# Kernel optimization log

Hardware: AMD Instinct MI355X
Metric: run time of the kernel (lower is better)

The kernel has to match this reference:

```python
import jax, jax.numpy as jnp
import numpy as np

B, L, G, D = 4096, 64, 8, 128
N_ITEMS, N_USERS, N_RATINGS = 100000, 50000, 5


def setup_inputs() -> dict:
    key = jax.random.key(0)
    ks = jax.random.split(key, 16)
    s = jnp.float32(0.02)
    return dict(
        nodes=jax.random.randint(ks[0], (B, G), 0, N_USERS),
        history_u=jax.random.randint(ks[1], (B, L), 0, N_ITEMS),
        history_r=jax.random.randint(ks[2], (B, L), 0, N_RATINGS),
        hist_len=jax.random.randint(ks[3], (B,), 0, L),
        v2e_weight=jax.random.normal(ks[4], (N_ITEMS, D), dtype=jnp.float32) * s,
        u2e_weight=jax.random.normal(ks[5], (N_USERS, D), dtype=jnp.float32) * s,
        r2e_weight=jax.random.normal(ks[6], (N_RATINGS, D), dtype=jnp.float32) * s,
        W1=jax.random.normal(ks[7], (2 * D, D), dtype=jnp.float32) * s,
        b1=jnp.zeros((D,), jnp.float32),
        W2=jax.random.normal(ks[8], (D, D), dtype=jnp.float32) * s,
        b2=jnp.zeros((D,), jnp.float32),
        att1_W=jax.random.normal(ks[9], (2 * D, D), dtype=jnp.float32) * s,
        att1_b=jnp.zeros((D,), jnp.float32),
        att2_W=jax.random.normal(ks[10], (D, D), dtype=jnp.float32) * s,
        att2_b=jnp.zeros((D,), jnp.float32),
        att3_W=jax.random.normal(ks[11], (D, 1), dtype=jnp.float32) * s,
        att3_b=jnp.zeros((1,), jnp.float32),
        ge_W=jax.random.normal(ks[12], (D, D), dtype=jnp.float32) * s,
        ge_b=jnp.zeros((D,), jnp.float32),
    )


def reference(nodes, history_u, history_r, hist_len,
              v2e_weight, u2e_weight, r2e_weight,
              W1, b1, W2, b2,
              att1_W, att1_b, att2_W, att2_b, att3_W, att3_b,
              ge_W, ge_b):
    lengths = hist_len + 1                      # ensure >=1 valid history entry per group
    e_uv = v2e_weight[history_u]                # [B, L, D] item-history gather
    e_r = r2e_weight[history_r]                 # [B, L, D] rating gather
    members = u2e_weight[nodes]                 # [B, G, D] member gather
    # Group_Embedding: pool members to one rep per group
    g = jax.nn.relu(members.mean(axis=1) @ ge_W + ge_b)            # [B, D]
    # per-history 2-layer MLP (w_r1, w_r2)
    x = jax.nn.relu(jnp.concatenate([e_uv, e_r], axis=-1) @ W1 + b1)
    o = jax.nn.relu(x @ W2 + b2)                # [B, L, D] o_history
    # Attention: cat(o_history, group_rep) -> relu -> relu -> scalar, softmax over L
    g_rep = jnp.broadcast_to(g[:, None, :], o.shape)               # [B, L, D]
    a = jax.nn.relu(jnp.concatenate([o, g_rep], axis=-1) @ att1_W + att1_b)
    a = jax.nn.relu(a @ att2_W + att2_b)
    logits = (a @ att3_W + att3_b)[..., 0]      # [B, L]
    mask = jnp.arange(L)[None, :] < lengths[:, None]
    logits = jnp.where(mask, logits, jnp.float32(-1e9))
    att = jax.nn.softmax(logits, axis=-1) * mask                   # ragged masked softmax
    # torch.mm(o_history.t(), att_w).t() == attention-weighted reduce over L
    return jnp.einsum('bl,bld->bd', att, o)     # [B, D]
```

## Files before the change

kernel.cpp:

```cpp
#include <hip/hip_runtime.h>
#include <hip/hip_bf16.h>

#define DD 128
#define TILE_BYTES 32768
#define WS_R_OFF   196608
#define WS_GB_OFF  199168

typedef __attribute__((ext_vector_type(8))) short bf16x8;
typedef __attribute__((ext_vector_type(4))) float f32x4;

__device__ inline unsigned short f2bf(float f) {
  unsigned u = __float_as_uint(f);
  return (unsigned short)((u + 0x7fffu + ((u >> 16) & 1u)) >> 16);
}
__device__ inline float bf2f(unsigned short h) {
  return __uint_as_float(((unsigned)h) << 16);
}

__device__ inline void async16(void* ldsp, const void* gp) {
  __builtin_amdgcn_global_load_lds(
      (const __attribute__((address_space(1))) void*)gp,
      (__attribute__((address_space(3))) void*)ldsp, 16, 0, 0);
}

__device__ inline void fill_w(char* slot, const char* src, int tid) {
  int w = tid >> 6, lane = tid & 63;
  #pragma unroll
  for (int i = 0; i < 8; ++i) {
    int ofs = ((i << 2) + w) << 10;
    async16(slot + ofs, src + ofs + lane * 16);
  }
}

__device__ inline bf16x8 ldfrag(const char* buf, int rowbase, int kk, int lane) {
  int row = rowbase + (lane & 15);
  int off = (row << 8) + (kk << 6) + (lane & 48);
  off ^= (row & 7) << 4;
  return *(const bf16x8*)(buf + off);
}

__device__ inline bf16x8 ldAg(const float* rp, int kk, int lane) {
  const float4* p = (const float4*)(rp + (kk << 5) + ((lane >> 4) << 3));
  float4 f0 = p[0], f1 = p[1];
  bf16x8 r;
  r[0] = (short)f2bf(f0.x); r[1] = (short)f2bf(f0.y);
  r[2] = (short)f2bf(f0.z); r[3] = (short)f2bf(f0.w);
  r[4] = (short)f2bf(f1.x); r[5] = (short)f2bf(f1.y);
  r[6] = (short)f2bf(f1.z); r[7] = (short)f2bf(f1.w);
  return r;
}

__device__ inline void gemm22(f32x4 acc[8], const char* A, const char* B,
                              int mi, int ni, int lane) {
  #pragma unroll
  for (int kk = 0; kk < 4; ++kk) {
    bf16x8 a0 = ldfrag(A, mi * 32, kk, lane);
    bf16x8 a1 = ldfrag(A, mi * 32 + 16, kk, lane);
    #pragma unroll
    for (int nf = 0; nf < 4; ++nf) {
      bf16x8 b = ldfrag(B, ni * 64 + nf * 16, kk, lane);
      acc[nf]     = __builtin_amdgcn_mfma_f32_16x16x32_bf16(a0, b, acc[nf], 0, 0, 0);
      acc[4 + nf] = __builtin_amdgcn_mfma_f32_16x16x32_bf16(a1, b, acc[4 + nf], 0, 0, 0);
    }
  }
}

__device__ inline void cwrite_col(char* buf, const f32x4 acc[8], const float bias4[4],
                                  int mi, int ni, int lane) {
  int cb = lane & 15, rb = (lane >> 4) << 2;
  #pragma unroll
  for (int mf = 0; mf < 2; ++mf)
    #pragma unroll
    for (int nf = 0; nf < 4; ++nf) {
      int col = ni * 64 + nf * 16 + cb;
      #pragma unroll
      for (int j = 0; j < 4; ++j) {
        int row = mi * 32 + mf * 16 + rb + j;
        float v = fmaxf(acc[mf * 4 + nf][j] + bias4[nf], 0.f);
        int off = ((row << 8) + (col << 1)) ^ ((row & 7) << 4);
        *(unsigned short*)(buf + off) = f2bf(v);
      }
    }
}

__global__ __launch_bounds__(256) void prep_weights(
    const float* __restrict__ W1, const float* __restrict__ W2,
    const float* __restrict__ a1W, const float* __restrict__ a2W,
    const float* __restrict__ geW,
    const float* __restrict__ r2e, const float* __restrict__ b1,
    unsigned short* __restrict__ wsw, float* __restrict__ Rp) {
  int gid = blockIdx.x * 256 + threadIdx.x;
  if (gid < 12288) {
    int tile = gid >> 11, idx = gid & 2047;
    int row = idx >> 4, slot = idx & 15;
    int slot2 = slot ^ (row & 7);
    const float* W; int kb;
    switch (tile) {
      case 0:  W = W1;  kb = 0;   break;
      case 1:  W = W2;  kb = 0;   break;
      case 2:  W = a1W; kb = 0;   break;
      case 3:  W = a2W; kb = 0;   break;
      case 4:  W = geW; kb = 0;   break;
      default: W = a1W; kb = 128; break;
    }
    unsigned pk[4];
    #pragma unroll
    for (int p = 0; p < 4; ++p) {
      unsigned short lo = f2bf(W[(size_t)(kb + slot2 * 8 + 2 * p) * DD + row]);
      unsigned short hi = f2bf(W[(size_t)(kb + slot2 * 8 + 2 * p + 1) * DD + row]);
      pk[p] = (unsigned)lo | ((unsigned)hi << 16);
    }
    *(uint4*)(wsw + (size_t)tile * 16384 + (size_t)idx * 8) =
        make_uint4(pk[0], pk[1], pk[2], pk[3]);
  } else {
    int t = gid - 12288;
    for (int idx = t; idx < 640; idx += 256) {
      int r = idx >> 7, d = idx & 127;
      float s = b1[d];
      for (int k = 0; k < 128; ++k)
        s = fmaf(r2e[r * DD + k], W1[(size_t)(DD + k) * DD + d], s);
      Rp[idx] = s;
    }
  }
}

__global__ __launch_bounds__(256, 2) void prep_gb(
    const int* __restrict__ nodes, const float* __restrict__ u2e,
    const float* __restrict__ geb, const float* __restrict__ a1b,
    const char* __restrict__ tiles, float* __restrict__ gbv) {
  __shared__ char mean_s[4096];
  __shared__ char g_s[4096];
  __shared__ char wslot[32768];
  __shared__ int nodes_s[128];
  int tid = threadIdx.x, w = tid >> 6, lane = tid & 63;
  int b0 = blockIdx.x * 16;
  if (tid < 128) nodes_s[tid] = nodes[b0 * 8 + tid];
  fill_w(wslot, tiles + 4 * TILE_BYTES, tid);
  __syncthreads();
  for (int idx = tid; idx < 2048; idx += 256) {
    int row = idx >> 7, d = idx & 127;
    float m = 0.f;
    #pragma unroll
    for (int j = 0; j < 8; ++j)
      m += u2e[(size_t)nodes_s[row * 8 + j] * DD + d];
    m *= 0.125f;
    int off = ((row << 8) + (d << 1)) ^ ((row & 7) << 4);
    *(unsigned short*)(mean_s + off) = f2bf(m);
  }
  __syncthreads();
  int cb = lane & 15, rb = (lane >> 4) << 2;
  f32x4 acc[2] = {(f32x4)(0.f), (f32x4)(0.f)};
  #pragma unroll
  for (int kk = 0; kk < 4; ++kk) {
    bf16x8 a = ldfrag(mean_s, 0, kk, lane);
    #pragma unroll
    for (int nf = 0; nf < 2; ++nf) {
      bf16x8 b = ldfrag(wslot, w * 32 + nf * 16, kk, lane);
      acc[nf] = __builtin_amdgcn_mfma_f32_16x16x32_bf16(a, b, acc[nf], 0, 0, 0);
    }
  }
  __syncthreads();
  fill_w(wslot, tiles + 5 * TILE_BYTES, tid);
  #pragma unroll
  for (int nf = 0; nf < 2; ++nf) {
    int col = w * 32 + nf * 16 + cb;
    float gb2 = geb[col];
    #pragma unroll
    for (int j = 0; j < 4; ++j) {
      int row = rb + j;
      float v = fmaxf(acc[nf][j] + gb2, 0.f);
      int off = ((row << 8) + (col << 1)) ^ ((row & 7) << 4);
      *(unsigned short*)(g_s + off) = f2bf(v);
    }
  }
  __syncthreads();
  acc[0] = (f32x4)(0.f); acc[1] = (f32x4)(0.f);
  #pragma unroll
  for (int kk = 0; kk < 4; ++kk) {
    bf16x8 a = ldfrag(g_s, 0, kk, lane);
    #pragma unroll
    for (int nf = 0; nf < 2; ++nf) {
      bf16x8 b = ldfrag(wslot, w * 32 + nf * 16, kk, lane);
      acc[nf] = __builtin_amdgcn_mfma_f32_16x16x32_bf16(a, b, acc[nf], 0, 0, 0);
    }
  }
  #pragma unroll
  for (int nf = 0; nf < 2; ++nf) {
    int col = w * 32 + nf * 16 + cb;
    float bb = a1b[col];
    #pragma unroll
    for (int j = 0; j < 4; ++j)
      gbv[(size_t)(b0 + rb + j) * DD + col] = acc[nf][j] + bb;
  }
}

__global__ __launch_bounds__(256, 2) void main_kernel(
    const int* __restrict__ hu, const int* __restrict__ hr,
    const int* __restrict__ hlen,
    const float* __restrict__ v2e,
    const float* __restrict__ b2, const float* __restrict__ a2b,
    const float* __restrict__ a3W, const float* __restrict__ a3b,
    const char* __restrict__ tiles, const float* __restrict__ Rp,
    const float* __restrict__ gbv, float* __restrict__ out) {
  __shared__ char X[16384];
  __shared__ char O[16384];
  __shared__ char W[32768];
  __shared__ float R_s[640];
  __shared__ int hu_s[64], hr_s[64];
  __shared__ float lpart[2][64];
  __shared__ float att_s[64];
  __shared__ float red_s[2][128];

  const int tid = threadIdx.x, w = tid >> 6, lane = tid & 63;
  const int mi = w >> 1, ni = w & 1;
  const int cb = lane & 15, rb = (lane >> 4) << 2;
  const int b0 = blockIdx.x;

  fill_w(W, tiles, tid);
  if (tid < 128) {
    int t = tid & 63;
    if (tid < 64) hu_s[t] = hu[b0 * 64 + t];
    else          hr_s[t] = hr[b0 * 64 + t];
  }
  for (int i = tid; i < 640; i += 256) R_s[i] = Rp[i];
  __syncthreads();

  f32x4 acc[8];
  #pragma unroll
  for (int i = 0; i < 8; ++i) acc[i] = (f32x4)(0.f);

  {
    const float* rp0 = v2e + (size_t)hu_s[mi * 32 + cb] * DD;
    const float* rp1 = v2e + (size_t)hu_s[mi * 32 + 16 + cb] * DD;
    #pragma unroll
    for (int kk = 0; kk < 4; ++kk) {
      bf16x8 a0 = ldAg(rp0, kk, lane);
      bf16x8 a1 = ldAg(rp1, kk, lane);
      #pragma unroll
      for (int nf = 0; nf < 4; ++nf) {
        bf16x8 b = ldfrag(W, ni * 64 + nf * 16, kk, lane);
        acc[nf]     = __builtin_amdgcn_mfma_f32_16x16x32_bf16(a0, b, acc[nf], 0, 0, 0);
        acc[4 + nf] = __builtin_amdgcn_mfma_f32_16x16x32_bf16(a1, b, acc[4 + nf], 0, 0, 0);
      }
    }
  }
  __syncthreads();
  fill_w(W, tiles + TILE_BYTES, tid);
  {
    int rat[2][4];
    #pragma unroll
    for (int mf = 0; mf < 2; ++mf)
      #pragma unroll
      for (int j = 0; j < 4; ++j)
        rat[mf][j] = hr_s[mi * 32 + mf * 16 + rb + j];
    #pragma unroll
    for (int mf = 0; mf < 2; ++mf)
      #pragma unroll
      for (int nf = 0; nf < 4; ++nf) {
        int col = ni * 64 + nf * 16 + cb;
        #pragma unroll
        for (int j = 0; j < 4; ++j) {
          int row = mi * 32 + mf * 16 + rb + j;
          float v = fmaxf(acc[mf * 4 + nf][j] + R_s[rat[mf][j] * DD + col], 0.f);
          int off = ((row << 8) + (col << 1)) ^ ((row & 7) << 4);
          *(unsigned short*)(X + off) = f2bf(v);
        }
      }
  }
  __syncthreads();

  #pragma unroll
  for (int i = 0; i < 8; ++i) acc[i] = (f32x4)(0.f);
  gemm22(acc, X, W, mi, ni, lane);
  __syncthreads();
  fill_w(W, tiles + 2 * TILE_BYTES, tid);
  {
    float bias4[4];
    #pragma unroll
    for (int nf = 0; nf < 4; ++nf) bias4[nf] = b2[ni * 64 + nf * 16 + cb];
    cwrite_col(O, acc, bias4, mi, ni, lane);
  }
  __syncthreads();

  #pragma unroll
  for (int i = 0; i < 8; ++i) acc[i] = (f32x4)(0.f);
  gemm22(acc, O, W, mi, ni, lane);
  __syncthreads();
  fill_w(W, tiles + 3 * TILE_BYTES, tid);
  {
    float bias4[4];
    #pragma unroll
    for (int nf = 0; nf < 4; ++nf)
      bias4[nf] = gbv[(size_t)b0 * DD + ni * 64 + nf * 16 + cb];
    cwrite_col(X, acc, bias4, mi, ni, lane);
  }
  __syncthreads();

  #pragma unroll
  for (int i = 0; i < 8; ++i) acc[i] = (f32x4)(0.f);
  gemm22(acc, X, W, mi, ni, lane);
  {
    float a2b4[4], a3w4[4];
    #pragma unroll
    for (int nf = 0; nf < 4; ++nf) {
      int col = ni * 64 + nf * 16 + cb;
      a2b4[nf] = a2b[col];
      a3w4[nf] = a3W[col];
    }
    float p[2][4];
    #pragma unroll
    for (int mf = 0; mf < 2; ++mf)
      #pragma unroll
      for (int j = 0; j < 4; ++j) {
        float s = 0.f;
        #pragma unroll
        for (int nf = 0; nf < 4; ++nf)
          s = fmaf(fmaxf(acc[mf * 4 + nf][j] + a2b4[nf], 0.f), a3w4[nf], s);
        p[mf][j] = s;
      }
    #pragma unroll
    for (int m = 1; m < 16; m <<= 1) {
      #pragma unroll
      for (int mf = 0; mf < 2; ++mf)
        #pragma unroll
        for (int j = 0; j < 4; ++j)
          p[mf][j] += __shfl_xor(p[mf][j], m);
    }
    if (cb == 0) {
      #pragma unroll
      for (int mf = 0; mf < 2; ++mf)
        #pragma unroll
        for (int j = 0; j < 4; ++j)
          lpart[ni][mi * 32 + mf * 16 + rb + j] = p[mf][j];
    }
  }
  __syncthreads();

  if (tid < 64) {
    float lv = lpart[0][tid] + lpart[1][tid] + a3b[0];
    int len = hlen[b0] + 1;
    bool valid = tid < len;
    if (!valid) lv = -1e30f;
    float m = lv;
    #pragma unroll
    for (int off = 32; off; off >>= 1) m = fmaxf(m, __shfl_xor(m, off));
    float pe = valid ? expf(lv - m) : 0.f;
    float s = pe;
    #pragma unroll
    for (int off = 32; off; off >>= 1) s += __shfl_xor(s, off);
    att_s[tid] = pe / s;
  }
  __syncthreads();

  {
    int d = tid & 127, h = tid >> 7;
    float s = 0.f;
    #pragma unroll 8
    for (int i = 0; i < 32; ++i) {
      int r = h * 32 + i;
      int off = ((r << 8) + (d << 1)) ^ ((r & 7) << 4);
      s = fmaf(att_s[r], bf2f(*(const unsigned short*)(O + off)), s);
    }
    red_s[h][d] = s;
  }
  __syncthreads();
  if (tid < 128)
    out[(size_t)b0 * DD + tid] = red_s[0][tid] + red_s[1][tid];
}

extern "C" void kernel_launch(void* const* d_in, const int* in_sizes, int n_in,
                              void* d_out, int out_size, void* d_ws, size_t ws_size,
                              hipStream_t stream) {
  const int*   nodes = (const int*)d_in[0];
  const int*   hu    = (const int*)d_in[1];
  const int*   hr    = (const int*)d_in[2];
  const int*   hlen  = (const int*)d_in[3];
  const float* v2e   = (const float*)d_in[4];
  const float* u2e   = (const float*)d_in[5];
  const float* r2e   = (const float*)d_in[6];
  const float* W1    = (const float*)d_in[7];
  const float* b1    = (const float*)d_in[8];
  const float* W2    = (const float*)d_in[9];
  const float* b2    = (const float*)d_in[10];
  const float* a1W   = (const float*)d_in[11];
  const float* a1b   = (const float*)d_in[12];
  const float* a2W   = (const float*)d_in[13];
  const float* a2b   = (const float*)d_in[14];
  const float* a3W   = (const float*)d_in[15];
  const float* a3b   = (const float*)d_in[16];
  const float* geW   = (const float*)d_in[17];
  const float* geb   = (const float*)d_in[18];
  float* out = (float*)d_out;

  unsigned short* wsw = (unsigned short*)d_ws;
  const char* tiles = (const char*)d_ws;
  float* Rp  = (float*)((char*)d_ws + WS_R_OFF);
  float* gbv = (float*)((char*)d_ws + WS_GB_OFF);

  prep_weights<<<49, 256, 0, stream>>>(W1, W2, a1W, a2W, geW, r2e, b1, wsw, Rp);
  prep_gb<<<256, 256, 0, stream>>>(nodes, u2e, geb, a1b, tiles, gbv);
  main_kernel<<<4096, 256, 0, stream>>>(
      hu, hr, hlen, v2e, b2, a2b, a3W, a3b, tiles, Rp, gbv, out);
}
```

Before: 127.5 us.

## Transpose MFMA roles so activations land feature-contiguous and keep o_history in registers

The GEMMs now compute W^T·X^T with weights as the A operand and history rows as B. Each lane then holds four consecutive features for one history row, so bias, rating-bias and ReLU epilogues write packed 8-byte bf16 stores and read float4 biases directly from global memory. The R_s/hu_s/hr_s/O shared buffers are removed and o_history is kept packed in registers for the final attention-weighted reduce, done with shuffles. Launch bounds are raised to 3 blocks per SM because less LDS is used. The cost is more register pressure and cross-lane shuffle reductions.

Measured after the change: 111.2 us. 1.15x faster.

```diff
diff --git a/kernel.cpp b/kernel.cpp
--- a/kernel.cpp
+++ b/kernel.cpp
@@ -12,9 +12,6 @@
 __device__ inline unsigned short f2bf(float f) {
   unsigned u = __float_as_uint(f);
   return (unsigned short)((u + 0x7fffu + ((u >> 16) & 1u)) >> 16);
-}
-__device__ inline float bf2f(unsigned short h) {
-  return __uint_as_float(((unsigned)h) << 16);
 }
 
 __device__ inline void async16(void* ldsp, const void* gp) {
@@ -50,38 +47,12 @@
   return r;
 }
 
-__device__ inline void gemm22(f32x4 acc[8], const char* A, const char* B,
-                              int mi, int ni, int lane) {
-  #pragma unroll
-  for (int kk = 0; kk < 4; ++kk) {
-    bf16x8 a0 = ldfrag(A, mi * 32, kk, lane);
-    bf16x8 a1 = ldfrag(A, mi * 32 + 16, kk, lane);
-    #pragma unroll
-    for (int nf = 0; nf < 4; ++nf) {
-      bf16x8 b = ldfrag(B, ni * 64 + nf * 16, kk, lane);
-      acc[nf]     = __builtin_amdgcn_mfma_f32_16x16x32_bf16(a0, b, acc[nf], 0, 0, 0);
-      acc[4 + nf] = __builtin_amdgcn_mfma_f32_16x16x32_bf16(a1, b, acc[4 + nf], 0, 0, 0);
-    }
-  }
-}
-
-__device__ inline void cwrite_col(char* buf, const f32x4 acc[8], const float bias4[4],
-                                  int mi, int ni, int lane) {
-  int cb = lane & 15, rb = (lane >> 4) << 2;
-  #pragma unroll
-  for (int mf = 0; mf < 2; ++mf)
-    #pragma unroll
-    for (int nf = 0; nf < 4; ++nf) {
-      int col = ni * 64 + nf * 16 + cb;
-      #pragma unroll
-      for (int j = 0; j < 4; ++j) {
-        int row = mi * 32 + mf * 16 + rb + j;
-        float v = fmaxf(acc[mf * 4 + nf][j] + bias4[nf], 0.f);
-        int off = ((row << 8) + (col << 1)) ^ ((row & 7) << 4);
-        *(unsigned short*)(buf + off) = f2bf(v);
-      }
-    }
-}
+__device__ inline uint2 pack4(float v0, float v1, float v2, float v3) {
+  return make_uint2((unsigned)f2bf(v0) | ((unsigned)f2bf(v1) << 16),
+                    (unsigned)f2bf(v2) | ((unsigned)f2bf(v3) << 16));
+}
+
+#define MFMA(a, b, c) __builtin_amdgcn_mfma_f32_16x16x32_bf16((a), (b), (c), 0, 0, 0)
 
 __global__ __launch_bounds__(256) void prep_weights(
     const float* __restrict__ W1, const float* __restrict__ W2,
@@ -156,7 +127,7 @@
     #pragma unroll
     for (int nf = 0; nf < 2; ++nf) {
       bf16x8 b = ldfrag(wslot, w * 32 + nf * 16, kk, lane);
-      acc[nf] = __builtin_amdgcn_mfma_f32_16x16x32_bf16(a, b, acc[nf], 0, 0, 0);
+      acc[nf] = MFMA(a, b, acc[nf]);
     }
   }
   __syncthreads();
@@ -181,7 +152,7 @@
     #pragma unroll
     for (int nf = 0; nf < 2; ++nf) {
       bf16x8 b = ldfrag(wslot, w * 32 + nf * 16, kk, lane);
-      acc[nf] = __builtin_amdgcn_mfma_f32_16x16x32_bf16(a, b, acc[nf], 0, 0, 0);
+      acc[nf] = MFMA(a, b, acc[nf]);
     }
   }
   #pragma unroll
@@ -194,7 +165,22 @@
   }
 }
 
-__global__ __launch_bounds__(256, 2) void main_kernel(
+__device__ inline void gemmWX(f32x4 acc[8], const char* Wt, const char* Xt,
+                              int mfw, int nlw, int lane) {
+  #pragma unroll
+  for (int kk = 0; kk < 4; ++kk) {
+    bf16x8 bf0 = ldfrag(Xt, nlw * 32, kk, lane);
+    bf16x8 bf1 = ldfrag(Xt, nlw * 32 + 16, kk, lane);
+    #pragma unroll
+    for (int mf = 0; mf < 4; ++mf) {
+      bf16x8 a = ldfrag(Wt, mfw * 64 + mf * 16, kk, lane);
+      acc[mf * 2]     = MFMA(a, bf0, acc[mf * 2]);
+      acc[mf * 2 + 1] = MFMA(a, bf1, acc[mf * 2 + 1]);
+    }
+  }
+}
+
+__global__ __launch_bounds__(256, 3) void main_kernel(
     const int* __restrict__ hu, const int* __restrict__ hr,
     const int* __restrict__ hlen,
     const float* __restrict__ v2e,
@@ -202,27 +188,22 @@
     const float* __restrict__ a3W, const float* __restrict__ a3b,
     const char* __restrict__ tiles, const float* __restrict__ Rp,
     const float* __restrict__ gbv, float* __restrict__ out) {
+  __shared__ char W[32768];
   __shared__ char X[16384];
-  __shared__ char O[16384];
-  __shared__ char W[32768];
-  __shared__ float R_s[640];
-  __shared__ int hu_s[64], hr_s[64];
   __shared__ float lpart[2][64];
   __shared__ float att_s[64];
   __shared__ float red_s[2][128];
 
-  const int tid = threadIdx.x, w = tid >> 6, lane = tid & 63;
-  const int mi = w >> 1, ni = w & 1;
-  const int cb = lane & 15, rb = (lane >> 4) << 2;
+  const int tid = threadIdx.x, lane = tid & 63;
+  const int wv = tid >> 6;
+  const int mfw = wv >> 1, nlw = wv & 1;
+  const int cb = lane & 15, g = lane >> 4;
   const int b0 = blockIdx.x;
 
   fill_w(W, tiles, tid);
-  if (tid < 128) {
-    int t = tid & 63;
-    if (tid < 64) hu_s[t] = hu[b0 * 64 + t];
-    else          hr_s[t] = hr[b0 * 64 + t];
-  }
-  for (int i = tid; i < 640; i += 256) R_s[i] = Rp[i];
+  const int l0 = nlw * 32 + cb, l1 = l0 + 16;
+  const int hu0 = hu[b0 * 64 + l0], hu1 = hu[b0 * 64 + l1];
+  const int hr0 = hr[b0 * 64 + l0], hr1 = hr[b0 * 64 + l1];
   __syncthreads();
 
   f32x4 acc[8];
@@ -230,109 +211,106 @@
   for (int i = 0; i < 8; ++i) acc[i] = (f32x4)(0.f);
 
   {
-    const float* rp0 = v2e + (size_t)hu_s[mi * 32 + cb] * DD;
-    const float* rp1 = v2e + (size_t)hu_s[mi * 32 + 16 + cb] * DD;
+    const float* rp0 = v2e + (size_t)hu0 * DD;
+    const float* rp1 = v2e + (size_t)hu1 * DD;
     #pragma unroll
     for (int kk = 0; kk < 4; ++kk) {
-      bf16x8 a0 = ldAg(rp0, kk, lane);
-      bf16x8 a1 = ldAg(rp1, kk, lane);
+      bf16x8 bf0 = ldAg(rp0, kk, lane);
+      bf16x8 bf1 = ldAg(rp1, kk, lane);
       #pragma unroll
-      for (int nf = 0; nf < 4; ++nf) {
-        bf16x8 b = ldfrag(W, ni * 64 + nf * 16, kk, lane);
-        acc[nf]     = __builtin_amdgcn_mfma_f32_16x16x32_bf16(a0, b, acc[nf], 0, 0, 0);
-        acc[4 + nf] = __builtin_amdgcn_mfma_f32_16x16x32_bf16(a1, b, acc[4 + nf], 0, 0, 0);
+      for (int mf = 0; mf < 4; ++mf) {
+        bf16x8 a = ldfrag(W, mfw * 64 + mf * 16, kk, lane);
+        acc[mf * 2]     = MFMA(a, bf0, acc[mf * 2]);
+        acc[mf * 2 + 1] = MFMA(a, bf1, acc[mf * 2 + 1]);
       }
     }
   }
   __syncthreads();
   fill_w(W, tiles + TILE_BYTES, tid);
+  #pragma unroll
+  for (int mf = 0; mf < 4; ++mf) {
+    int f0 = mfw * 64 + mf * 16 + g * 4;
+    float4 r0 = *(const float4*)(Rp + hr0 * DD + f0);
+    float4 r1 = *(const float4*)(Rp + hr1 * DD + f0);
+    f32x4 v0 = acc[mf * 2], v1 = acc[mf * 2 + 1];
+    uint2 p0 = pack4(fmaxf(v0[0] + r0.x, 0.f), fmaxf(v0[1] + r0.y, 0.f),
+                     fmaxf(v0[2] + r0.z, 0.f), fmaxf(v0[3] + r0.w, 0.f));
+    uint2 p1 = pack4(fmaxf(v1[0] + r1.x, 0.f), fmaxf(v1[1] + r1.y, 0.f),
+                     fmaxf(v1[2] + r1.z, 0.f), fmaxf(v1[3] + r1.w, 0.f));
+    int o0 = ((l0 << 8) + (f0 << 1)) ^ ((l0 & 7) << 4);
+    int o1 = ((l1 << 8) + (f0 << 1)) ^ ((l1 & 7) << 4);
+    *(uint2*)(X + o0) = p0;
+    *(uint2*)(X + o1) = p1;
+  }
+  __syncthreads();
+
+  #pragma unroll
+  for (int i = 0; i < 8; ++i) acc[i] = (f32x4)(0.f);
+  gemmWX(acc, W, X, mfw, nlw, lane);
+  __syncthreads();
+  fill_w(W, tiles + 2 * TILE_BYTES, tid);
+  uint2 opk[8];
+  #pragma unroll
+  for (int mf = 0; mf < 4; ++mf) {
+    int f0 = mfw * 64 + mf * 16 + g * 4;
+    float4 bb = *(const float4*)(b2 + f0);
+    f32x4 v0 = acc[mf * 2], v1 = acc[mf * 2 + 1];
+    uint2 p0 = pack4(fmaxf(v0[0] + bb.x, 0.f), fmaxf(v0[1] + bb.y, 0.f),
+                     fmaxf(v0[2] + bb.z, 0.f), fmaxf(v0[3] + bb.w, 0.f));
+    uint2 p1 = pack4(fmaxf(v1[0] + bb.x, 0.f), fmaxf(v1[1] + bb.y, 0.f),
+                     fmaxf(v1[2] + bb.z, 0.f), fmaxf(v1[3] + bb.w, 0.f));
+    opk[mf * 2] = p0; opk[mf * 2 + 1] = p1;
+    int o0 = ((l0 << 8) + (f0 << 1)) ^ ((l0 & 7) << 4);
+    int o1 = ((l1 << 8) + (f0 << 1)) ^ ((l1 & 7) << 4);
+    *(uint2*)(X + o0) = p0;
+    *(uint2*)(X + o1) = p1;
+  }
+  __syncthreads();
+
+  #pragma unroll
+  for (int i = 0; i < 8; ++i) acc[i] = (f32x4)(0.f);
+  gemmWX(acc, W, X, mfw, nlw, lane);
+  __syncthreads();
+  fill_w(W, tiles + 3 * TILE_BYTES, tid);
+  #pragma unroll
+  for (int mf = 0; mf < 4; ++mf) {
+    int f0 = mfw * 64 + mf * 16 + g * 4;
+    float4 gg = *(const float4*)(gbv + (size_t)b0 * DD + f0);
+    f32x4 v0 = acc[mf * 2], v1 = acc[mf * 2 + 1];
+    uint2 p0 = pack4(fmaxf(v0[0] + gg.x, 0.f), fmaxf(v0[1] + gg.y, 0.f),
+                     fmaxf(v0[2] + gg.z, 0.f), fmaxf(v0[3] + gg.w, 0.f));
+    uint2 p1 = pack4(fmaxf(v1[0] + gg.x, 0.f), fmaxf(v1[1] + gg.y, 0.f),
+                     fmaxf(v1[2] + gg.z, 0.f), fmaxf(v1[3] + gg.w, 0.f));
+    int o0 = ((l0 << 8) + (f0 << 1)) ^ ((l0 & 7) << 4);
+    int o1 = ((l1 << 8) + (f0 << 1)) ^ ((l1 & 7) << 4);
+    *(uint2*)(X + o0) = p0;
+    *(uint2*)(X + o1) = p1;
+  }
+  __syncthreads();
+
+  #pragma unroll
+  for (int i = 0; i < 8; ++i) acc[i] = (f32x4)(0.f);
+  gemmWX(acc, W, X, mfw, nlw, lane);
   {
-    int rat[2][4];
-    #pragma unroll
-    for (int mf = 0; mf < 2; ++mf)
-      #pragma unroll
-      for (int j = 0; j < 4; ++j)
-        rat[mf][j] = hr_s[mi * 32 + mf * 16 + rb + j];
-    #pragma unroll
-    for (int mf = 0; mf < 2; ++mf)
-      #pragma unroll
-      for (int nf = 0; nf < 4; ++nf) {
-        int col = ni * 64 + nf * 16 + cb;
-        #pragma unroll
-        for (int j = 0; j < 4; ++j) {
-          int row = mi * 32 + mf * 16 + rb + j;
-          float v = fmaxf(acc[mf * 4 + nf][j] + R_s[rat[mf][j] * DD + col], 0.f);
-          int off = ((row << 8) + (col << 1)) ^ ((row & 7) << 4);
-          *(unsigned short*)(X + off) = f2bf(v);
-        }
-      }
-  }
-  __syncthreads();
-
-  #pragma unroll
-  for (int i = 0; i < 8; ++i) acc[i] = (f32x4)(0.f);
-  gemm22(acc, X, W, mi, ni, lane);
-  __syncthreads();
-  fill_w(W, tiles + 2 * TILE_BYTES, tid);
-  {
-    float bias4[4];
-    #pragma unroll
-    for (int nf = 0; nf < 4; ++nf) bias4[nf] = b2[ni * 64 + nf * 16 + cb];
-    cwrite_col(O, acc, bias4, mi, ni, lane);
-  }
-  __syncthreads();
-
-  #pragma unroll
-  for (int i = 0; i < 8; ++i) acc[i] = (f32x4)(0.f);
-  gemm22(acc, O, W, mi, ni, lane);
-  __syncthreads();
-  fill_w(W, tiles + 3 * TILE_BYTES, tid);
-  {
-    float bias4[4];
-    #pragma unroll
-    for (int nf = 0; nf < 4; ++nf)
-      bias4[nf] = gbv[(size_t)b0 * DD + ni * 64 + nf * 16 + cb];
-    cwrite_col(X, acc, bias4, mi, ni, lane);
-  }
-  __syncthreads();
-
-  #pragma unroll
-  for (int i = 0; i < 8; ++i) acc[i] = (f32x4)(0.f);
-  gemm22(acc, X, W, mi, ni, lane);
-  {
-    float a2b4[4], a3w4[4];
-    #pragma unroll
-    for (int nf = 0; nf < 4; ++nf) {
-      int col = ni * 64 + nf * 16 + cb;
-      a2b4[nf] = a2b[col];
-      a3w4[nf] = a3W[col];
-    }
-    float p[2][4];
-    #pragma unroll
-    for (int mf = 0; mf < 2; ++mf)
-      #pragma unroll
-      for (int j = 0; j < 4; ++j) {
-        float s = 0.f;
-        #pragma unroll
-        for (int nf = 0; nf < 4; ++nf)
-          s = fmaf(fmaxf(acc[mf * 4 + nf][j] + a2b4[nf], 0.f), a3w4[nf], s);
-        p[mf][j] = s;
-      }
-    #pragma unroll
-    for (int m = 1; m < 16; m <<= 1) {
-      #pragma unroll
-      for (int mf = 0; mf < 2; ++mf)
-        #pragma unroll
-        for (int j = 0; j < 4; ++j)
-          p[mf][j] += __shfl_xor(p[mf][j], m);
-    }
-    if (cb == 0) {
-      #pragma unroll
-      for (int mf = 0; mf < 2; ++mf)
-        #pragma unroll
-        for (int j = 0; j < 4; ++j)
-          lpart[ni][mi * 32 + mf * 16 + rb + j] = p[mf][j];
-    }
+    float s0 = 0.f, s1 = 0.f;
+    #pragma unroll
+    for (int mf = 0; mf < 4; ++mf) {
+      int f0 = mfw * 64 + mf * 16 + g * 4;
+      float4 ab = *(const float4*)(a2b + f0);
+      float4 aw = *(const float4*)(a3W + f0);
+      f32x4 v0 = acc[mf * 2], v1 = acc[mf * 2 + 1];
+      s0 = fmaf(fmaxf(v0[0] + ab.x, 0.f), aw.x, s0);
+      s0 = fmaf(fmaxf(v0[1] + ab.y, 0.f), aw.y, s0);
+      s0 = fmaf(fmaxf(v0[2] + ab.z, 0.f), aw.z, s0);
+      s0 = fmaf(fmaxf(v0[3] + ab.w, 0.f), aw.w, s0);
+      s1 = fmaf(fmaxf(v1[0] + ab.x, 0.f), aw.x, s1);
+      s1 = fmaf(fmaxf(v1[1] + ab.y, 0.f), aw.y, s1);
+      s1 = fmaf(fmaxf(v1[2] + ab.z, 0.f), aw.z, s1);
+      s1 = fmaf(fmaxf(v1[3] + ab.w, 0.f), aw.w, s1);
+    }
+    s0 += __shfl_xor(s0, 16); s0 += __shfl_xor(s0, 32);
+    s1 += __shfl_xor(s1, 16); s1 += __shfl_xor(s1, 32);
+    if (g == 0) { lpart[mfw][l0] = s0; lpart[mfw][l1] = s1; }
   }
   __syncthreads();
 
@@ -353,15 +331,40 @@
   __syncthreads();
 
   {
-    int d = tid & 127, h = tid >> 7;
-    float s = 0.f;
-    #pragma unroll 8
-    for (int i = 0; i < 32; ++i) {
-      int r = h * 32 + i;
-      int off = ((r << 8) + (d << 1)) ^ ((r & 7) << 4);
-      s = fmaf(att_s[r], bf2f(*(const unsigned short*)(O + off)), s);
-    }
-    red_s[h][d] = s;
+    float att0 = att_s[l0], att1 = att_s[l1];
+    float p[4][4];
+    #pragma unroll
+    for (int mf = 0; mf < 4; ++mf) {
+      uint2 q0 = opk[mf * 2], q1 = opk[mf * 2 + 1];
+      p[mf][0] = att0 * __uint_as_float(q0.x << 16)
+               + att1 * __uint_as_float(q1.x << 16);
+      p[mf][1] = att0 * __uint_as_float(q0.x & 0xffff0000u)
+               + att1 * __uint_as_float(q1.x & 0xffff0000u);
+      p[mf][2] = att0 * __uint_as_float(q0.y << 16)
+               + att1 * __uint_as_float(q1.y << 16);
+      p[mf][3] = att0 * __uint_as_float(q0.y & 0xffff0000u)
+               + att1 * __uint_as_float(q1.y & 0xffff0000u);
+    }
+    #pragma unroll
+    for (int m = 1; m < 16; m <<= 1) {
+      #pragma unroll
+      for (int mf = 0; mf < 4; ++mf) {
+        p[mf][0] += __shfl_xor(p[mf][0], m);
+        p[mf][1] += __shfl_xor(p[mf][1], m);
+        p[mf][2] += __shfl_xor(p[mf][2], m);
+        p[mf][3] += __shfl_xor(p[mf][3], m);
+      }
+    }
+    if (cb == 0) {
+      #pragma unroll
+      for (int mf = 0; mf < 4; ++mf) {
+        int d = mfw * 64 + mf * 16 + g * 4;
+        red_s[nlw][d + 0] = p[mf][0];
+        red_s[nlw][d + 1] = p[mf][1];
+        red_s[nlw][d + 2] = p[mf][2];
+        red_s[nlw][d + 3] = p[mf][3];
+      }
+    }
   }
   __syncthreads();
   if (tid < 128)
```
